# Kernel tuning notes

Hardware: AMD Instinct MI355X
Metric: run time of the kernel (lower is better)

The kernel has to match this reference:

```python
import jax, jax.numpy as jnp
import numpy as np

BITS = 4
MAXQ = (1 << BITS) - 1      # 15
PACK = 32 // BITS           # 8 values per int32 word
GROUP = 128                 # quantization group size along K


def setup_inputs() -> dict:
    key = jax.random.key(0)
    k0, k1, k2, k3 = jax.random.split(key, 4)
    M, K, N = 4096, 4096, 11008
    G = K // GROUP
    x = jax.random.normal(k0, (M, K), dtype=jnp.float32)
    # packed 4-bit weights: full-range random int32 words (each holds 8 nibbles)
    qweight = jax.random.randint(k1, (K // PACK, N), -(2**31), 2**31 - 1, dtype=jnp.int32)
    # packed zero points: (G, N // PACK) int32 words
    qzeros = jax.random.randint(k2, (G, N // PACK), -(2**31), 2**31 - 1, dtype=jnp.int32)
    # group-wise scales (G, N), small positive values as GPTQ produces
    scales = jax.random.uniform(k3, (G, N), dtype=jnp.float32, minval=1e-3, maxval=1e-2)
    # standard GPTQ grouping: consecutive blocks of GROUP rows share a group
    g_idx = (jnp.arange(K) // GROUP).astype(jnp.int32)
    return {"x": x, "qweight": qweight, "scales": scales, "qzeros": qzeros, "g_idx": g_idx}


def _dequant(qweight, scales, qzeros, g_idx):
    """Unpack int32-packed 4-bit weights and dequantize to float. Returns (K, N)."""
    K = g_idx.shape[0]
    N = qweight.shape[1]
    k = jnp.arange(K)
    # nibble k lives in word k//PACK at bit offset (k%PACK)*BITS
    k_shift = ((k % PACK) * BITS).astype(jnp.int32)
    w = (qweight[k // PACK] >> k_shift[:, None]) & MAXQ              # (K, N) int32 in [0, MAXQ]
    n = jnp.arange(N)
    n_shift = ((n % PACK) * BITS).astype(jnp.int32)
    z = ((qzeros[:, n // PACK] >> n_shift[None, :]) & MAXQ) + 1      # (G, N); kernel adds 1
    return (w - z[g_idx]).astype(scales.dtype) * scales[g_idx]       # (K, N) float


def reference(x, qweight, scales, qzeros, g_idx):
    # C = A @ dequant(B), fp32 accumulation as in the Triton kernel
    W = _dequant(qweight, scales, qzeros, g_idx)
    return jnp.matmul(x, W, preferred_element_type=jnp.float32)
```

## Files before the change

kernel.cpp:

```cpp
#include <hip/hip_runtime.h>
#include <hip/hip_bf16.h>
#include <stdint.h>

typedef __attribute__((ext_vector_type(8))) short short8;
typedef __attribute__((ext_vector_type(4))) float floatx4;

#define BM 128
#define BN 128
#define BK 64
#define NTHREADS 256
#define GROUP_SZ 128

__device__ __forceinline__ uint32_t cvt_pk_bf16(float lo, float hi) {
    uint32_t r;
    asm("v_cvt_pk_bf16_f32 %0, %1, %2" : "=v"(r) : "v"(lo), "v"(hi));
    return r;
}

__device__ __forceinline__ uint32_t swz(uint32_t row, uint32_t byte_in_row) {
    return row * 128u + (byte_in_row ^ ((row & 7u) << 4));
}

__global__ __launch_bounds__(NTHREADS, 2)
void gptq_gemm_kernel(const float* __restrict__ x,
                      const int* __restrict__ qweight,
                      const float* __restrict__ scales,
                      const int* __restrict__ qzeros,
                      float* __restrict__ out,
                      int M, int K, int N) {
    __shared__ char smem[(BM * BK + BN * BK) * 2];
    char* Ald = smem;
    char* Bld = smem + BM * BK * 2;

    const int nbm = M / BM, nbn = N / BN;
    const int nwg = nbm * nbn;
    int bid = blockIdx.x;
    int q = nwg >> 3, r = nwg & 7;
    int xcd = bid & 7, lin = bid >> 3;
    int sid = (xcd < r ? xcd * (q + 1) : r * (q + 1) + (xcd - r) * q) + lin;
    int bm = sid / nbn, bn = sid % nbn;
    const int m0 = bm * BM, n0 = bn * BN;

    const int t = threadIdx.x;
    const int lane = t & 63, wave = t >> 6;

    const int tm = t >> 4;
    const int tk4 = t & 15;
    const int sn = t & 127;
    const int kwh = t >> 7;

    const int gn = n0 + sn;
    const int NT = K / BK;

    float4 av[8];
    uint32_t qw[4];
    float sc, nz;

    auto load_tile = [&](int ts) {
        const int k0 = ts * BK;
        const float* xb = x + (size_t)(m0 + tm) * K + k0 + tk4 * 4;
        #pragma unroll
        for (int i = 0; i < 8; ++i)
            av[i] = *reinterpret_cast<const float4*>(xb + (size_t)i * 16 * K);
        const int g = k0 >> 7;
        sc = scales[(size_t)g * N + gn];
        const uint32_t zw = (uint32_t)qzeros[(size_t)g * (N >> 3) + (gn >> 3)];
        const float z = (float)((zw >> ((gn & 7) * 4)) & 15u) + 1.0f;
        nz = -z * sc;
        const int* qb = qweight + (size_t)((k0 >> 3) + kwh * 4) * N + gn;
        #pragma unroll
        for (int j = 0; j < 4; ++j)
            qw[j] = (uint32_t)qb[(size_t)j * N];
    };

    auto write_tile = [&]() {
        #pragma unroll
        for (int i = 0; i < 8; ++i) {
            uint2 p;
            p.x = cvt_pk_bf16(av[i].x, av[i].y);
            p.y = cvt_pk_bf16(av[i].z, av[i].w);
            *reinterpret_cast<uint2*>(Ald + swz((uint32_t)(i * 16 + tm), (uint32_t)(tk4 * 8))) = p;
        }
        #pragma unroll
        for (int j = 0; j < 4; ++j) {
            const uint32_t w = qw[j];
            float f[8];
            #pragma unroll
            for (int e = 0; e < 8; ++e)
                f[e] = fmaf((float)((w >> (4 * e)) & 15u), sc, nz);
            uint4 p;
            p.x = cvt_pk_bf16(f[0], f[1]);
            p.y = cvt_pk_bf16(f[2], f[3]);
            p.z = cvt_pk_bf16(f[4], f[5]);
            p.w = cvt_pk_bf16(f[6], f[7]);
            *reinterpret_cast<uint4*>(Bld + swz((uint32_t)sn, (uint32_t)((kwh * 4 + j) * 16))) = p;
        }
    };

    floatx4 acc[4][4];
    const floatx4 fzero = {0.f, 0.f, 0.f, 0.f};
    #pragma unroll
    for (int i = 0; i < 4; ++i)
        #pragma unroll
        for (int j = 0; j < 4; ++j)
            acc[i][j] = fzero;

    const int wm = (wave >> 1) * 64, wn = (wave & 1) * 64;
    const int fr = lane & 15;
    const int fkb = ((lane >> 4) * 8) * 2;

    auto compute = [&]() {
        #pragma unroll
        for (int kk = 0; kk < 2; ++kk) {
            short8 af[4], bf[4];
            #pragma unroll
            for (int i = 0; i < 4; ++i)
                af[i] = *reinterpret_cast<const short8*>(
                    Ald + swz((uint32_t)(wm + i * 16 + fr), (uint32_t)(kk * 64 + fkb)));
            #pragma unroll
            for (int i = 0; i < 4; ++i)
                bf[i] = *reinterpret_cast<const short8*>(
                    Bld + swz((uint32_t)(wn + i * 16 + fr), (uint32_t)(kk * 64 + fkb)));
            #pragma unroll
            for (int i = 0; i < 4; ++i)
                #pragma unroll
                for (int j = 0; j < 4; ++j)
                    acc[i][j] = __builtin_amdgcn_mfma_f32_16x16x32_bf16(af[i], bf[j], acc[i][j], 0, 0, 0);
        }
    };

    load_tile(0);
    write_tile();
    __syncthreads();
    for (int ts = 0; ts < NT; ++ts) {
        if (ts + 1 < NT) load_tile(ts + 1);
        compute();
        __syncthreads();
        if (ts + 1 < NT) write_tile();
        __syncthreads();
    }

    const int fq = lane >> 4;
    float* op = out + (size_t)(m0 + wm) * N + n0 + wn;
    #pragma unroll
    for (int i = 0; i < 4; ++i)
        #pragma unroll
        for (int j = 0; j < 4; ++j)
            #pragma unroll
            for (int rr = 0; rr < 4; ++rr)
                op[(size_t)(i * 16 + fq * 4 + rr) * N + j * 16 + fr] = acc[i][j][rr];
}

extern "C" void kernel_launch(void* const* d_in, const int* in_sizes, int n_in,
                              void* d_out, int out_size, void* d_ws, size_t ws_size,
                              hipStream_t stream) {
    const float* x       = (const float*)d_in[0];
    const int*   qweight = (const int*)d_in[1];
    const float* scales  = (const float*)d_in[2];
    const int*   qzeros  = (const int*)d_in[3];

    const int K = in_sizes[4];
    const int M = in_sizes[0] / K;
    const int G = K / GROUP_SZ;
    const int N = in_sizes[2] / G;
    float* out = (float*)d_out;

    const int nwg = (M / BM) * (N / BN);
    hipLaunchKernelGGL(gptq_gemm_kernel, dim3(nwg), dim3(NTHREADS), 0, stream,
                       x, qweight, scales, qzeros, out, M, K, N);
}
```

Baseline: 476.5 us.

## Switch to fp16 MFMA with magic-number dequant and double-buffered LDS

Moves the operands from bf16 to fp16 and dequantizes the 4-bit weights with the 0x6400 magic-bias trick plus packed f16 add and mul, replacing per-element int-to-float conversion and fma. It also double-buffers the LDS tiles so each k-step needs one barrier instead of two, and it loads scales and zeros only once per quantization group with incremented pointers. This trades bf16's range for fp16 precision on the activations, and doubles shared memory use, which may lower occupancy.

```diff
diff --git a/kernel.cpp b/kernel.cpp
--- a/kernel.cpp
+++ b/kernel.cpp
@@ -2,23 +2,35 @@
 #include <hip/hip_bf16.h>
 #include <stdint.h>
 
-typedef __attribute__((ext_vector_type(8))) short short8;
+typedef _Float16 half8 __attribute__((ext_vector_type(8)));
 typedef __attribute__((ext_vector_type(4))) float floatx4;
+typedef __attribute__((ext_vector_type(4))) uint32_t uint32x4;
 
 #define BM 128
 #define BN 128
 #define BK 64
 #define NTHREADS 256
 #define GROUP_SZ 128
-
-__device__ __forceinline__ uint32_t cvt_pk_bf16(float lo, float hi) {
-    uint32_t r;
-    asm("v_cvt_pk_bf16_f32 %0, %1, %2" : "=v"(r) : "v"(lo), "v"(hi));
-    return r;
-}
+#define TILE_B (BM * BK * 2)
 
 __device__ __forceinline__ uint32_t swz(uint32_t row, uint32_t byte_in_row) {
     return row * 128u + (byte_in_row ^ ((row & 7u) << 4));
+}
+
+__device__ __forceinline__ uint32_t cvt_pk_f16(float lo, float hi) {
+    uint32_t r;
+    asm("v_cvt_pkrtz_f16_f32 %0, %1, %2" : "=v"(r) : "v"(lo), "v"(hi));
+    return r;
+}
+__device__ __forceinline__ uint32_t pk_add_f16(uint32_t a, uint32_t b) {
+    uint32_t r;
+    asm("v_pk_add_f16 %0, %1, %2" : "=v"(r) : "v"(a), "v"(b));
+    return r;
+}
+__device__ __forceinline__ uint32_t pk_mul_f16(uint32_t a, uint32_t b) {
+    uint32_t r;
+    asm("v_pk_mul_f16 %0, %1, %2" : "=v"(r) : "v"(a), "v"(b));
+    return r;
 }
 
 __global__ __launch_bounds__(NTHREADS, 2)
@@ -28,9 +40,7 @@
                       const int* __restrict__ qzeros,
                       float* __restrict__ out,
                       int M, int K, int N) {
-    __shared__ char smem[(BM * BK + BN * BK) * 2];
-    char* Ald = smem;
-    char* Bld = smem + BM * BK * 2;
+    __shared__ char smem[2 * 2 * TILE_B];
 
     const int nbm = M / BM, nbn = N / BN;
     const int nwg = nbm * nbn;
@@ -52,47 +62,56 @@
     const int gn = n0 + sn;
     const int NT = K / BK;
 
+    const float* xp = x + (size_t)(m0 + tm) * K + tk4 * 4;
+    const int*   qp = qweight + (size_t)(kwh * 4) * N + gn;
+    const float* sp = scales + gn;
+    const int*   zp = qzeros + (gn >> 3);
+    const int    zsh = (gn & 7) * 4;
+
     float4 av[8];
     uint32_t qw[4];
-    float sc, nz;
+    float sc;
+    uint32_t zw;
 
     auto load_tile = [&](int ts) {
-        const int k0 = ts * BK;
-        const float* xb = x + (size_t)(m0 + tm) * K + k0 + tk4 * 4;
         #pragma unroll
         for (int i = 0; i < 8; ++i)
-            av[i] = *reinterpret_cast<const float4*>(xb + (size_t)i * 16 * K);
-        const int g = k0 >> 7;
-        sc = scales[(size_t)g * N + gn];
-        const uint32_t zw = (uint32_t)qzeros[(size_t)g * (N >> 3) + (gn >> 3)];
-        const float z = (float)((zw >> ((gn & 7) * 4)) & 15u) + 1.0f;
-        nz = -z * sc;
-        const int* qb = qweight + (size_t)((k0 >> 3) + kwh * 4) * N + gn;
+            av[i] = *reinterpret_cast<const float4*>(xp + (size_t)i * 16 * K);
+        xp += BK;
         #pragma unroll
         for (int j = 0; j < 4; ++j)
-            qw[j] = (uint32_t)qb[(size_t)j * N];
+            qw[j] = (uint32_t)qp[(size_t)j * N];
+        qp += (size_t)(BK / 8) * N;
+        if ((ts & 1) == 0) {
+            const int g = ts >> 1;
+            sc = sp[(size_t)g * N];
+            zw = (uint32_t)zp[(size_t)g * (N >> 3)];
+        }
     };
 
-    auto write_tile = [&]() {
+    auto write_tile = [&](char* Ald, char* Bld) {
         #pragma unroll
         for (int i = 0; i < 8; ++i) {
             uint2 p;
-            p.x = cvt_pk_bf16(av[i].x, av[i].y);
-            p.y = cvt_pk_bf16(av[i].z, av[i].w);
+            p.x = cvt_pk_f16(av[i].x, av[i].y);
+            p.y = cvt_pk_f16(av[i].z, av[i].w);
             *reinterpret_cast<uint2*>(Ald + swz((uint32_t)(i * 16 + tm), (uint32_t)(tk4 * 8))) = p;
         }
+        const float zf = -(float)(1025u + ((zw >> zsh) & 15u));
+        const uint32_t c2 = cvt_pk_f16(zf, zf);
+        const uint32_t s2 = cvt_pk_f16(sc, sc);
         #pragma unroll
         for (int j = 0; j < 4; ++j) {
             const uint32_t w = qw[j];
-            float f[8];
+            uint32_t o[4];
             #pragma unroll
-            for (int e = 0; e < 8; ++e)
-                f[e] = fmaf((float)((w >> (4 * e)) & 15u), sc, nz);
+            for (int i = 0; i < 4; ++i) {
+                const uint32_t tt = w >> (8 * i);
+                const uint32_t qi = ((tt & 0xFu) | 0x64006400u) | ((tt << 12) & 0xF0000u);
+                o[i] = pk_mul_f16(pk_add_f16(qi, c2), s2);
+            }
             uint4 p;
-            p.x = cvt_pk_bf16(f[0], f[1]);
-            p.y = cvt_pk_bf16(f[2], f[3]);
-            p.z = cvt_pk_bf16(f[4], f[5]);
-            p.w = cvt_pk_bf16(f[6], f[7]);
+            p.x = o[0]; p.y = o[1]; p.z = o[2]; p.w = o[3];
             *reinterpret_cast<uint4*>(Bld + swz((uint32_t)sn, (uint32_t)((kwh * 4 + j) * 16))) = p;
         }
     };
@@ -109,35 +128,43 @@
     const int fr = lane & 15;
     const int fkb = ((lane >> 4) * 8) * 2;
 
-    auto compute = [&]() {
+    auto compute = [&](const char* Ald, const char* Bld) {
         #pragma unroll
         for (int kk = 0; kk < 2; ++kk) {
-            short8 af[4], bf[4];
+            half8 af[4], bf[4];
             #pragma unroll
-            for (int i = 0; i < 4; ++i)
-                af[i] = *reinterpret_cast<const short8*>(
+            for (int i = 0; i < 4; ++i) {
+                uint32x4 u = *reinterpret_cast<const uint32x4*>(
                     Ald + swz((uint32_t)(wm + i * 16 + fr), (uint32_t)(kk * 64 + fkb)));
+                af[i] = __builtin_bit_cast(half8, u);
+            }
             #pragma unroll
-            for (int i = 0; i < 4; ++i)
-                bf[i] = *reinterpret_cast<const short8*>(
+            for (int i = 0; i < 4; ++i) {
+                uint32x4 u = *reinterpret_cast<const uint32x4*>(
                     Bld + swz((uint32_t)(wn + i * 16 + fr), (uint32_t)(kk * 64 + fkb)));
+                bf[i] = __builtin_bit_cast(half8, u);
+            }
             #pragma unroll
             for (int i = 0; i < 4; ++i)
                 #pragma unroll
                 for (int j = 0; j < 4; ++j)
-                    acc[i][j] = __builtin_amdgcn_mfma_f32_16x16x32_bf16(af[i], bf[j], acc[i][j], 0, 0, 0);
+                    acc[i][j] = __builtin_amdgcn_mfma_f32_16x16x32_f16(af[i], bf[j], acc[i][j], 0, 0, 0);
         }
     };
 
     load_tile(0);
-    write_tile();
-    __syncthreads();
+    write_tile(smem, smem + TILE_B);
+    int cur = 0;
     for (int ts = 0; ts < NT; ++ts) {
+        __syncthreads();
         if (ts + 1 < NT) load_tile(ts + 1);
-        compute();
-        __syncthreads();
-        if (ts + 1 < NT) write_tile();
-        __syncthreads();
+        char* base = smem + cur * (2 * TILE_B);
+        compute(base, base + TILE_B);
+        if (ts + 1 < NT) {
+            char* nbase = smem + (cur ^ 1) * (2 * TILE_B);
+            write_tile(nbase, nbase + TILE_B);
+        }
+        cur ^= 1;
     }
 
     const int fq = lane >> 4;
```

Result: slower. 542.5 us (+13.9%).
